# Performance work log

Measured on AMD Instinct MI355X. Metric: run time of the kernel, lower is better.

The kernel has to match this reference:

```python
import jax, jax.numpy as jnp
import numpy as np

BATCH, MAXPV = 32, 50
RULENUM, PROPNUM = 256, 256  # must be equal (eye(rulenum) * property_importance)
ENT_DIM, RULE_DIM = 128, 128
ENTITYNUM = 50000
THRESHOLD = 0.5


def _l2norm(x, eps=1e-12):
    # F.normalize(p=2, dim=-1)
    n = jnp.linalg.norm(x, axis=-1, keepdims=True)
    return x / jnp.clip(n, eps)


def setup_inputs() -> dict:
    key = jax.random.key(0)
    ks = jax.random.split(key, 20)
    d_in = ENT_DIM + RULE_DIM
    inp = {
        'property': jax.random.randint(ks[0], (BATCH, MAXPV), 0, ENTITYNUM),
        'value': jax.random.randint(ks[1], (BATCH, MAXPV), 0, ENTITYNUM),
        'samemask': jax.random.randint(ks[2], (BATCH, MAXPV), 0, 2),
        'padmask': jax.random.randint(ks[3], (BATCH, MAXPV), 0, 2),
        'rule_embedding': jax.random.normal(ks[4], (RULENUM, RULE_DIM), jnp.float32),
        'entity_table': jax.random.normal(ks[5], (ENTITYNUM, ENT_DIM), jnp.float32),
        # Linear weights stored (in, out); concat order in the original is (p_emb, rule_emb)
        'fc1_w': jax.random.normal(ks[6], (d_in, ENT_DIM), jnp.float32),
        'fc1_b': jax.random.normal(ks[7], (ENT_DIM,), jnp.float32) * 0.02,
        'fc2_w': jax.random.normal(ks[8], (d_in, ENT_DIM), jnp.float32),
        'fc2_b': jax.random.normal(ks[9], (ENT_DIM,), jnp.float32) * 0.02,
        'fc3_w': jax.random.normal(ks[10], (d_in, ENT_DIM), jnp.float32),
        'fc3_b': jax.random.normal(ks[11], (ENT_DIM,), jnp.float32) * 0.02,
        'fc4_w': jax.random.normal(ks[12], (ENT_DIM, 1), jnp.float32) * 0.05,
        'fc4_b': jax.random.normal(ks[13], (1,), jnp.float32) * 0.02,
        'fc5_w': jax.random.normal(ks[14], (ENT_DIM, 1), jnp.float32) * 0.05,
        'fc5_b': jax.random.normal(ks[15], (1,), jnp.float32) * 0.02,
        'fc6_w': jax.random.normal(ks[16], (ENT_DIM, ENT_DIM), jnp.float32) * 0.05,
        'fc6_b': jax.random.normal(ks[17], (ENT_DIM,), jnp.float32) * 0.02,
    }
    return inp


def reference(property, value, samemask, padmask, rule_embedding, entity_table,
              fc1_w, fc1_b, fc2_w, fc2_b, fc3_w, fc3_b,
              fc4_w, fc4_b, fc5_w, fc5_b, fc6_w, fc6_b):
    E = entity_table.shape[1]
    R = rule_embedding.shape[0]
    P = R  # propertynum == rulenum (required by eye() regularizer)

    p_emb = _l2norm(entity_table[property])   # (B, M, E)
    v_emb = _l2norm(entity_table[value])      # (B, M, E)
    r_emb = _l2norm(rule_embedding)           # (R, Dr)

    # cat(p, rule) -> Linear decomposed into two smaller matmuls (same math)
    def branch(w, b):
        return p_emb @ w[:E], r_emb @ w[E:] + b  # (B,M,Eo), (R,Eo)

    # s1 branch
    pa, ra = branch(fc1_w, fc1_b)
    h1 = jax.nn.relu(pa[:, None, :, :] + ra[None, :, None, :])   # (B,R,M,E)
    s1 = jax.nn.sigmoid(h1 @ fc4_w + fc4_b)[..., 0]              # (B,R,M)

    # p branch
    pb, rb = branch(fc2_w, fc2_b)
    h2 = jax.nn.relu(pb[:, None, :, :] + rb[None, :, None, :])
    p = jax.nn.sigmoid(h2 @ fc5_w + fc5_b)[..., 0]               # (B,R,M)

    # s2 branch
    pc, rc = branch(fc3_w, fc3_b)
    h3 = jax.nn.relu(pc[:, None, :, :] + rc[None, :, None, :])
    gv = _l2norm(h3 @ fc6_w + fc6_b)                             # (B,R,M,E)
    vb = v_emb[:, None, :, :]                                    # (B,1,M,E)
    denom = jnp.clip(jnp.linalg.norm(vb, axis=-1) * jnp.linalg.norm(gv, axis=-1), 1e-8)
    cos = jnp.sum(vb * gv, axis=-1) / denom
    s2 = 0.5 * cos + 0.5                                         # (B,R,M)

    score = p + (1.0 - p) * s2
    score = jnp.where(samemask[:, None, :] == 1, s1 * score, 1.0 - s1)

    # property importance K: fc1/fc4 on cat(prop_emb, rule_emb)
    prop_emb = _l2norm(entity_table[:P])                         # propertyids = arange(P)
    pi_h = jax.nn.relu((prop_emb @ fc1_w[:E])[None, :, :]
                       + (r_emb @ fc1_w[E:] + fc1_b)[:, None, :])  # (R,P,E)
    pi = jax.nn.sigmoid(pi_h @ fc4_w + fc4_b)[..., 0]            # (R,P)

    rule_mask = jnp.sum(pi * (pi > THRESHOLD), axis=-1) + 1.0    # (R,)

    score = score * padmask[:, None, :].astype(score.dtype)
    score = score * (s1 > THRESHOLD)
    score = jnp.sum(score, axis=-1) / rule_mask[None, :]          # (B,R)
    pooledscore = jnp.max(score, axis=1)                          # (B,)

    diag = jnp.eye(R, dtype=pi.dtype)
    reg = pi * diag + (1.0 - pi) * (1.0 - diag)
    reg = -jnp.log(reg + 1e-8) * (1.0 - diag + diag * R)
    reg_logits = jnp.mean(reg)
    return pooledscore, reg_logits
```

## Files before the change

### kernel.cpp

```cpp
#include <hip/hip_runtime.h>
#include <hip/hip_bf16.h>

#define BATCH 32
#define MAXPV 50
#define RN 256
#define PN 256
#define DIM 128
#define NPV (BATCH*MAXPV*DIM)
#define NI (BATCH*MAXPV)

typedef unsigned short u16;
typedef __attribute__((ext_vector_type(8))) short short8;
typedef __attribute__((ext_vector_type(4))) float f32x4;

__device__ float g_p[NPV], g_v[NPV], g_pa[NPV], g_pb[NPV], g_pc[NPV];
__device__ float g_ra[RN*DIM], g_rb[RN*DIM], g_rc[RN*DIM], g_pp1[PN*DIM];
__device__ float g_prop[PN*DIM], g_re[RN*DIM];
__device__ float g_raT[DIM*RN], g_rbT[DIM*RN];
__device__ float2 g_s1p[NI*RN];
__device__ float g_piv[PN*RN];
__device__ float g_rmask[RN], g_regp[RN];
__device__ float g_scores[(size_t)NI*RN];
__device__ short8 g_bfrag[8][4][64];
__device__ float g_rcA[16*4*64*8];
__device__ int   g_ftype, g_i64;

__device__ __forceinline__ float bf2f(u16 u){ return __uint_as_float(((unsigned)u)<<16); }
__device__ __forceinline__ float LD(const void* p, size_t i){
    return g_ftype ? bf2f(((const u16*)p)[i]) : ((const float*)p)[i];
}
__device__ __forceinline__ int LDI(const void* p, size_t i){
    return g_i64 ? (int)((const long long*)p)[i] : ((const int*)p)[i];
}
__device__ __forceinline__ short f2bf(float f){
    unsigned u = __float_as_uint(f);
    u = (u + 0x7FFFu + ((u>>16)&1u)) >> 16;
    return (short)u;
}
__device__ __forceinline__ float wred(float v){
#pragma unroll
    for(int o=32;o;o>>=1) v += __shfl_xor(v,o,64);
    return v;
}
__device__ __forceinline__ double wredd(double v){
#pragma unroll
    for(int o=32;o;o>>=1) v += __shfl_xor(v,o,64);
    return v;
}
__device__ __forceinline__ float wmax(float v){
#pragma unroll
    for(int o=32;o;o>>=1) v = fmaxf(v,__shfl_xor(v,o,64));
    return v;
}

__global__ void k_detect(const u16* __restrict__ ent, const unsigned* __restrict__ prop){
    __shared__ int c[2];
    int t = threadIdx.x;
    if(t<2) c[t]=0;
    __syncthreads();
    int ee = (ent[2*(size_t)t*977]>>7)&0xFF;
    if(ee>=120 && ee<=133) atomicAdd(&c[0],1);
    if(t<32 && prop[2*t+1]==0u) atomicAdd(&c[1],1);
    __syncthreads();
    if(t==0){ g_ftype = (c[0]>=200)?1:0; g_i64 = (c[1]>=30)?1:0; }
}

__global__ void k_norm(const void* __restrict__ ent, const void* __restrict__ rule,
                       const void* __restrict__ prop, const void* __restrict__ val){
    int row = blockIdx.x*4 + (threadIdx.x>>6);
    int l = threadIdx.x & 63;
    const void* src; size_t off; float* dst;
    if(row < 1600){ src=ent; off=(size_t)LDI(prop,row)*DIM; dst=g_p+(size_t)row*DIM; }
    else if(row < 3200){ int i=row-1600; src=ent; off=(size_t)LDI(val,i)*DIM; dst=g_v+(size_t)i*DIM; }
    else if(row < 3456){ int i=row-3200; src=rule; off=(size_t)i*DIM; dst=g_re+(size_t)i*DIM; }
    else { int i=row-3456; src=ent; off=(size_t)i*DIM; dst=g_prop+(size_t)i*DIM; }
    float a = LD(src,off+l), b = LD(src,off+l+64);
    float n = fmaxf(sqrtf((float)wredd((double)a*a+(double)b*b)), 1e-12f);
    dst[l]=a/n; dst[l+64]=b/n;
}

__global__ __launch_bounds__(256) void k_mm(
    const void* __restrict__ fc1w, const void* __restrict__ fc2w, const void* __restrict__ fc3w,
    const void* __restrict__ fc1b, const void* __restrict__ fc2b, const void* __restrict__ fc3b){
    __shared__ float s_w[64*DIM];
    __shared__ float s_in[16*DIM];
    __shared__ float s_bias[DIM];
    const int blk = blockIdx.x, tid = threadIdx.x;
    const float* in; const void* w; size_t woff=0; const void* bptr=nullptr; float* out; int row0;
    if(blk < 100){ row0=blk*16; in=g_p; w=fc1w; out=g_pa; }
    else if(blk < 200){ row0=(blk-100)*16; in=g_p; w=fc2w; out=g_pb; }
    else if(blk < 300){ row0=(blk-200)*16; in=g_p; w=fc3w; out=g_pc; }
    else if(blk < 316){ row0=(blk-300)*16; in=g_re; w=fc1w; woff=DIM*DIM; bptr=fc1b; out=g_ra; }
    else if(blk < 332){ row0=(blk-316)*16; in=g_re; w=fc2w; woff=DIM*DIM; bptr=fc2b; out=g_rb; }
    else if(blk < 348){ row0=(blk-332)*16; in=g_re; w=fc3w; woff=DIM*DIM; bptr=fc3b; out=g_rc; }
    else { row0=(blk-348)*16; in=g_prop; w=fc1w; out=g_pp1; }
    for(int t=tid; t<16*DIM; t+=256) s_in[t] = in[(size_t)row0*DIM + t];
    if(tid<DIM) s_bias[tid] = bptr ? LD(bptr,tid) : 0.f;
    const int j = tid & 127;
    const int rb8 = (tid>>7)*8;
    double acc[8] = {0,0,0,0,0,0,0,0};
    for(int half=0; half<2; half++){
        __syncthreads();
        for(int t=tid; t<64*DIM; t+=256)
            s_w[t] = LD(w, woff + (size_t)(half*64 + (t>>7))*DIM + (t&127));
        __syncthreads();
        for(int k=0;k<64;k++){
            float wk = s_w[k*DIM + j];
#pragma unroll
            for(int rr=0;rr<8;rr++)
                acc[rr] += (double)s_in[(rb8+rr)*DIM + half*64 + k]*(double)wk;
        }
    }
    const double bj = (double)s_bias[j];
#pragma unroll
    for(int rr=0;rr<8;rr++) out[(size_t)(row0+rb8+rr)*DIM + j] = (float)(bj + acc[rr]);
}

__global__ void k_prep(const void* __restrict__ fc6w){
    int blk = blockIdx.x, tid = threadIdx.x;
    if(blk < 64){
        int idx0 = blk*256 + tid;
#pragma unroll
        for(int n=0;n<4;n++){
            int idx = idx0 + n*16384;
            int which = idx>>15;
            int k = (idx>>8)&127, r = idx&255;
            if(which) g_rbT[k*256+r] = g_rb[(size_t)r*DIM+k];
            else      g_raT[k*256+r] = g_ra[(size_t)r*DIM+k];
        }
    } else if(blk < 72){
        int nt = blk-64;
        int ks = tid>>6, lane = tid&63;
        int n = nt*16 + (lane&15);
        int k0 = ks*32 + (lane>>4)*8;
        short8 v;
#pragma unroll
        for(int j=0;j<8;j++) v[j] = f2bf(LD(fc6w,(size_t)(k0+j)*DIM + n));
        g_bfrag[nt][ks][lane] = v;
    } else {
        for(int idx=tid; idx<4096; idx+=256){
            int mt = (blk-72)*2 + (idx>>11);
            int rem = idx & 2047;
            int ks = rem>>9;
            int lane = (rem>>3)&63;
            int j = rem&7;
            int am = lane&15, quad = lane>>4;
            g_rcA[((mt*4+ks)*64+lane)*8 + j] =
                g_rc[(size_t)(mt*16+am)*DIM + ks*32 + quad*8 + j];
        }
    }
}

__global__ __launch_bounds__(256) void k_gate(
    const void* __restrict__ fc4w, const void* __restrict__ fc4b,
    const void* __restrict__ fc5w, const void* __restrict__ fc5b){
    __shared__ float s_a[4][DIM], s_b[4][DIM], s_f5[DIM];
    __shared__ double s_f4[DIM];
    const int blk = blockIdx.x, tid = threadIdx.x;
    const bool typeA = blk < 400;
    const int i0 = typeA ? blk*4 : (blk-400)*4;
    if(tid<DIM){ s_f4[tid]=(double)LD(fc4w,tid); s_f5[tid]=LD(fc5w,tid); }
    for(int t=tid; t<4*DIM; t+=256){
        int ii=t>>7, k=t&127;
        s_a[ii][k] = typeA ? g_pa[(size_t)(i0+ii)*DIM+k] : g_pp1[(size_t)(i0+ii)*DIM+k];
        if(typeA) s_b[ii][k] = g_pb[(size_t)(i0+ii)*DIM+k];
    }
    __syncthreads();
    const int r = tid;
    double d[4]={0.0,0.0,0.0,0.0}; float pq[4]={0.f,0.f,0.f,0.f};
    if(typeA){
        for(int k=0;k<DIM;k++){
            float rav = g_raT[k*256+r];
            float rbv = g_rbT[k*256+r];
            double f4k = s_f4[k]; float f5k = s_f5[k];
#pragma unroll
            for(int ii=0;ii<4;ii++){
                d[ii] += (double)fmaxf(s_a[ii][k]+rav,0.f)*f4k;
                pq[ii] = fmaf(fmaxf(s_b[ii][k]+rbv,0.f), f5k, pq[ii]);
            }
        }
    } else {
        for(int k=0;k<DIM;k++){
            float rav = g_raT[k*256+r];
            double f4k = s_f4[k];
#pragma unroll
            for(int ii=0;ii<4;ii++)
                d[ii] += (double)fmaxf(s_a[ii][k]+rav,0.f)*f4k;
        }
    }
    const double b4 = (double)LD(fc4b,0);
    const float b5 = LD(fc5b,0);
#pragma unroll
    for(int ii=0;ii<4;ii++){
        double sd = d[ii] + b4;
        bool gate = sd > 0.0;
        float s1v = 1.f/(1.f+expf(-(float)sd));
        if(typeA){
            float p = 1.f/(1.f+expf(-(pq[ii] + b5)));
            float2 o; o.x = gate ? s1v : -s1v; o.y = p;
            g_s1p[(size_t)(i0+ii)*RN + r] = o;
        } else {
            g_piv[(size_t)(i0+ii)*RN + r] = gate ? s1v : -s1v;
        }
    }
}

__global__ void k_pired(){
    const int r = blockIdx.x, tid = threadIdx.x;
    float v = g_piv[(size_t)tid*RN + r];
    float piv = fabsf(v);
    float m = (v > 0.f) ? piv : 0.f;
    float eff = (tid==r) ? piv : (1.f - piv);
    float wgt = (tid==r) ? (float)RN : 1.f;
    float rg = -logf(eff + 1e-8f)*wgt;
    int w = tid>>6, l = tid&63;
    m = wred(m); rg = wred(rg);
    __shared__ float sm[4], sg[4];
    if(l==0){ sm[w]=m; sg[w]=rg; }
    __syncthreads();
    if(tid==0){
        g_rmask[r] = 1.f + sm[0]+sm[1]+sm[2]+sm[3];
        g_regp[r]  = sg[0]+sg[1]+sg[2]+sg[3];
    }
}

__global__ __launch_bounds__(256) void k_main(
    const void* __restrict__ fc6b,
    const void* __restrict__ same, const void* __restrict__ pad){
    const int blk = blockIdx.x;
    const int i = blk >> 1, h = blk & 1;
    if(LDI(same,i)!=1 || LDI(pad,i)!=1) return;
    __shared__ float s_pc[DIM];
    __shared__ float s_st[128][4][2];
    const int tid = threadIdx.x, w = tid>>6, l = tid&63;
    const int am = l&15, quad = l>>4;

    if(tid < DIM) s_pc[tid] = g_pc[(size_t)i*DIM + tid];

    short8 bA[4], bB[4];
#pragma unroll
    for(int ks=0; ks<4; ks++){ bA[ks]=g_bfrag[2*w][ks][l]; bB[ks]=g_bfrag[2*w+1][ks][l]; }
    const int n0 = w*32 + am, n1 = n0 + 16;
    const float v0 = g_v[(size_t)i*DIM + n0], v1 = g_v[(size_t)i*DIM + n1];
    const float b60 = LD(fc6b, n0), b61 = LD(fc6b, n1);

    float vl = g_v[(size_t)i*DIM + l], vh = g_v[(size_t)i*DIM + l + 64];
    const float nvb = sqrtf(wred(vl*vl + vh*vh));
    __syncthreads();

    int mt = h*8;
    float4 c[8];
#pragma unroll
    for(int ks=0; ks<4; ks++){
        const float* rp = &g_rcA[((mt*4+ks)*64 + l)*8];
        c[2*ks]   = *(const float4*)rp;
        c[2*ks+1] = *(const float4*)(rp+4);
    }
    for(int mtl=0; mtl<8; mtl++){
        float4 n[8];
        if(mtl < 7){
#pragma unroll
            for(int ks=0; ks<4; ks++){
                const float* rp = &g_rcA[(((mt+1)*4+ks)*64 + l)*8];
                n[2*ks]   = *(const float4*)rp;
                n[2*ks+1] = *(const float4*)(rp+4);
            }
        }
        short8 a[4];
#pragma unroll
        for(int ks=0; ks<4; ks++){
            const float4 p0 = *(const float4*)&s_pc[ks*32 + quad*8];
            const float4 p1 = *(const float4*)&s_pc[ks*32 + quad*8 + 4];
            const float4 c0 = c[2*ks], c1 = c[2*ks+1];
            short8 t;
            t[0]=f2bf(fmaxf(p0.x+c0.x,0.f)); t[1]=f2bf(fmaxf(p0.y+c0.y,0.f));
            t[2]=f2bf(fmaxf(p0.z+c0.z,0.f)); t[3]=f2bf(fmaxf(p0.w+c0.w,0.f));
            t[4]=f2bf(fmaxf(p1.x+c1.x,0.f)); t[5]=f2bf(fmaxf(p1.y+c1.y,0.f));
            t[6]=f2bf(fmaxf(p1.z+c1.z,0.f)); t[7]=f2bf(fmaxf(p1.w+c1.w,0.f));
            a[ks]=t;
        }
        f32x4 acc0 = {0.f,0.f,0.f,0.f}, acc1 = {0.f,0.f,0.f,0.f};
#pragma unroll
        for(int ks=0; ks<4; ks++){
            acc0 = __builtin_amdgcn_mfma_f32_16x16x32_bf16(a[ks], bA[ks], acc0, 0,0,0);
            acc1 = __builtin_amdgcn_mfma_f32_16x16x32_bf16(a[ks], bB[ks], acc1, 0,0,0);
        }
#pragma unroll
        for(int q=0; q<4; q++){
            float x0 = acc0[q] + b60;
            float x1 = acc1[q] + b61;
            float ss = x0*x0 + x1*x1;
            float dv = x0*v0 + x1*v1;
#pragma unroll
            for(int o=1;o<16;o<<=1){ ss += __shfl_xor(ss,o,64); dv += __shfl_xor(dv,o,64); }
            if(am==0){
                int row = mtl*16 + quad*4 + q;
                s_st[row][w][0] = ss;
                s_st[row][w][1] = dv;
            }
        }
#pragma unroll
        for(int x=0;x<8;x++) c[x] = n[x];
        mt++;
    }
    __syncthreads();
    if(tid < 128){
        const int r = h*128 + tid;
        float ss = s_st[tid][0][0]+s_st[tid][1][0]+s_st[tid][2][0]+s_st[tid][3][0];
        float dv = s_st[tid][0][1]+s_st[tid][1][1]+s_st[tid][2][1]+s_st[tid][3][1];
        float2 sp = g_s1p[(size_t)i*RN + r];
        float s1 = fabsf(sp.x);
        float gate = (sp.x > 0.f) ? 1.f : 0.f;
        float pp = sp.y;
        float nx = sqrtf(ss);
        float clipnx = fmaxf(nx, 1e-12f);
        float gvn = nx/clipnx;
        float denom = fmaxf(nvb*gvn, 1e-8f);
        float cosv = (dv/clipnx)/denom;
        float s2 = 0.5f*cosv + 0.5f;
        float sc = s1*(pp + (1.f-pp)*s2);
        g_scores[(size_t)i*RN + r] = sc * gate;
    }
}

__global__ void k_fin(float* __restrict__ out,
                      const void* __restrict__ same, const void* __restrict__ pad){
    const int blk = blockIdx.x, tid = threadIdx.x;
    const int w = tid>>6, l = tid&63;
    __shared__ float s[4];
    if(blk < 32){
        __shared__ int s_same[MAXPV], s_pad[MAXPV];
        if(tid < MAXPV){
            s_same[tid] = LDI(same, (size_t)blk*MAXPV + tid);
            s_pad[tid]  = LDI(pad,  (size_t)blk*MAXPV + tid);
        }
        __syncthreads();
        float ssum = 0.f;
        for(int pv=0; pv<MAXPV; pv++){
            if(!s_pad[pv]) continue;
            const size_t i = (size_t)blk*MAXPV + pv;
            if(s_same[pv]==1) ssum += g_scores[i*RN + tid];
            else { float sx = g_s1p[i*RN + tid].x; ssum += (sx > 0.f) ? (1.f - sx) : 0.f; }
        }
        float sc = ssum / g_rmask[tid];
        float m = wmax(sc);
        if(l==0) s[w]=m;
        __syncthreads();
        if(tid==0) out[blk] = fmaxf(fmaxf(s[0],s[1]), fmaxf(s[2],s[3]));
    } else {
        float v = g_regp[tid];
        v = wred(v);
        if(l==0) s[w]=v;
        __syncthreads();
        if(tid==0) out[32] = (s[0]+s[1]+s[2]+s[3]) / (float)(RN*PN);
    }
}

extern "C" void kernel_launch(void* const* d_in, const int* in_sizes, int n_in,
                              void* d_out, int out_size, void* d_ws, size_t ws_size,
                              hipStream_t stream){
    int map[18]; for(int i=0;i<18;i++) map[i]=i;
    if(n_in>=18 && in_sizes[0]==6400000){
        const int a[18] = {14,17,16,13,15,0,2,1,4,3,6,5,8,7,10,9,12,11};
        for(int i=0;i<18;i++) map[i]=a[i];
    }
    const void* prop = d_in[map[0]];
    const void* val  = d_in[map[1]];
    const void* same = d_in[map[2]];
    const void* pad  = d_in[map[3]];
    const void* rule = d_in[map[4]];
    const void* ent  = d_in[map[5]];
    const void* fc1w = d_in[map[6]];
    const void* fc1b = d_in[map[7]];
    const void* fc2w = d_in[map[8]];
    const void* fc2b = d_in[map[9]];
    const void* fc3w = d_in[map[10]];
    const void* fc3b = d_in[map[11]];
    const void* fc4w = d_in[map[12]];
    const void* fc4b = d_in[map[13]];
    const void* fc5w = d_in[map[14]];
    const void* fc5b = d_in[map[15]];
    const void* fc6w = d_in[map[16]];
    const void* fc6b = d_in[map[17]];

    k_detect<<<1, 256, 0, stream>>>((const u16*)ent, (const unsigned*)prop);
    k_norm<<<928, 256, 0, stream>>>(ent, rule, prop, val);
    k_mm<<<364, 256, 0, stream>>>(fc1w, fc2w, fc3w, fc1b, fc2b, fc3b);
    k_prep<<<80, 256, 0, stream>>>(fc6w);
    k_gate<<<464, 256, 0, stream>>>(fc4w, fc4b, fc5w, fc5b);
    k_pired<<<RN, 256, 0, stream>>>();
    k_main<<<NI*2, 256, 0, stream>>>(fc6b, same, pad);
    k_fin<<<33, 256, 0, stream>>>((float*)d_out, same, pad);
}
```

Measured before the change: 217.6 us.

## Fold detect, prep and pi-reduction kernels into neighbours to cut launches

Removes the separate detect, prep and pired kernels. Dtype detection now runs per wave through a ballot inside each kernel, the fc6 fragment packing moves into extra k_norm blocks, and k_mm writes the transposed and MFMA-packed rule outputs directly. The rule-mask and regularizer reductions become atomicAdds inside k_gate, and bf16 conversion uses a packed intrinsic. This cuts eight launches to five and drops the intermediate buffers, in exchange for redundant detection loads in every block, atomic contention on 256 addresses, and a float sum order that now depends on atomic ordering.

```diff
diff --git a/kernel.cpp b/kernel.cpp
--- a/kernel.cpp
+++ b/kernel.cpp
@@ -14,29 +14,42 @@
 typedef __attribute__((ext_vector_type(4))) float f32x4;
 
 __device__ float g_p[NPV], g_v[NPV], g_pa[NPV], g_pb[NPV], g_pc[NPV];
-__device__ float g_ra[RN*DIM], g_rb[RN*DIM], g_rc[RN*DIM], g_pp1[PN*DIM];
-__device__ float g_prop[PN*DIM], g_re[RN*DIM];
+__device__ float g_pp1[PN*DIM], g_prop[PN*DIM], g_re[RN*DIM];
 __device__ float g_raT[DIM*RN], g_rbT[DIM*RN];
 __device__ float2 g_s1p[NI*RN];
-__device__ float g_piv[PN*RN];
 __device__ float g_rmask[RN], g_regp[RN];
 __device__ float g_scores[(size_t)NI*RN];
 __device__ short8 g_bfrag[8][4][64];
 __device__ float g_rcA[16*4*64*8];
-__device__ int   g_ftype, g_i64;
 
 __device__ __forceinline__ float bf2f(u16 u){ return __uint_as_float(((unsigned)u)<<16); }
-__device__ __forceinline__ float LD(const void* p, size_t i){
-    return g_ftype ? bf2f(((const u16*)p)[i]) : ((const float*)p)[i];
-}
-__device__ __forceinline__ int LDI(const void* p, size_t i){
-    return g_i64 ? (int)((const long long*)p)[i] : ((const int*)p)[i];
+__device__ __forceinline__ float LD(const void* p, size_t i, bool bf){
+    return bf ? bf2f(((const u16*)p)[i]) : ((const float*)p)[i];
+}
+__device__ __forceinline__ int LDI(const void* p, size_t i, bool w64){
+    return w64 ? (int)((const long long*)p)[i] : ((const int*)p)[i];
 }
 __device__ __forceinline__ short f2bf(float f){
     unsigned u = __float_as_uint(f);
     u = (u + 0x7FFFu + ((u>>16)&1u)) >> 16;
     return (short)u;
 }
+__device__ __forceinline__ unsigned f2bf2(float x, float y){
+    float2 f; f.x=x; f.y=y;
+    __hip_bfloat162 h = __float22bfloat162_rn(f);
+    union { __hip_bfloat162 h; unsigned u; } c; c.h=h; return c.u;
+}
+__device__ __forceinline__ bool det_bf16(const void* ent){
+    int l = threadIdx.x & 63;
+    u16 v = ((const u16*)ent)[(size_t)2*(l*4)*977];
+    int e = (v>>7)&0xFF;
+    return __popcll(__ballot(e>=120 && e<=133)) >= 48;
+}
+__device__ __forceinline__ bool det_i64(const void* prop){
+    int l = threadIdx.x & 63;
+    bool z = (l<32) ? (((const unsigned*)prop)[2*l+1]==0u) : false;
+    return __popcll(__ballot(z)) >= 30;
+}
 __device__ __forceinline__ float wred(float v){
 #pragma unroll
     for(int o=32;o;o>>=1) v += __shfl_xor(v,o,64);
@@ -53,56 +66,63 @@
     return v;
 }
 
-__global__ void k_detect(const u16* __restrict__ ent, const unsigned* __restrict__ prop){
-    __shared__ int c[2];
-    int t = threadIdx.x;
-    if(t<2) c[t]=0;
-    __syncthreads();
-    int ee = (ent[2*(size_t)t*977]>>7)&0xFF;
-    if(ee>=120 && ee<=133) atomicAdd(&c[0],1);
-    if(t<32 && prop[2*t+1]==0u) atomicAdd(&c[1],1);
-    __syncthreads();
-    if(t==0){ g_ftype = (c[0]>=200)?1:0; g_i64 = (c[1]>=30)?1:0; }
-}
-
 __global__ void k_norm(const void* __restrict__ ent, const void* __restrict__ rule,
-                       const void* __restrict__ prop, const void* __restrict__ val){
-    int row = blockIdx.x*4 + (threadIdx.x>>6);
-    int l = threadIdx.x & 63;
+                       const void* __restrict__ prop, const void* __restrict__ val,
+                       const void* __restrict__ fc6w){
+    const bool bf = det_bf16(ent);
+    const int blk = blockIdx.x, tid = threadIdx.x;
+    if(blk >= 928){
+        int nt = blk-928;
+        int ks = tid>>6, lane = tid&63;
+        int n = nt*16 + (lane&15);
+        int k0 = ks*32 + (lane>>4)*8;
+        short8 v;
+#pragma unroll
+        for(int j=0;j<8;j++) v[j] = f2bf(LD(fc6w,(size_t)(k0+j)*DIM + n, bf));
+        g_bfrag[nt][ks][lane] = v;
+        if(nt==0){ g_rmask[tid] = 1.f; g_regp[tid] = 0.f; }
+        return;
+    }
+    const bool w64 = det_i64(prop);
+    int row = blk*4 + (tid>>6);
+    int l = tid & 63;
     const void* src; size_t off; float* dst;
-    if(row < 1600){ src=ent; off=(size_t)LDI(prop,row)*DIM; dst=g_p+(size_t)row*DIM; }
-    else if(row < 3200){ int i=row-1600; src=ent; off=(size_t)LDI(val,i)*DIM; dst=g_v+(size_t)i*DIM; }
+    if(row < 1600){ src=ent; off=(size_t)LDI(prop,row,w64)*DIM; dst=g_p+(size_t)row*DIM; }
+    else if(row < 3200){ int i=row-1600; src=ent; off=(size_t)LDI(val,i,w64)*DIM; dst=g_v+(size_t)i*DIM; }
     else if(row < 3456){ int i=row-3200; src=rule; off=(size_t)i*DIM; dst=g_re+(size_t)i*DIM; }
     else { int i=row-3456; src=ent; off=(size_t)i*DIM; dst=g_prop+(size_t)i*DIM; }
-    float a = LD(src,off+l), b = LD(src,off+l+64);
+    float a = LD(src,off+l,bf), b = LD(src,off+l+64,bf);
     float n = fmaxf(sqrtf((float)wredd((double)a*a+(double)b*b)), 1e-12f);
     dst[l]=a/n; dst[l+64]=b/n;
 }
 
 __global__ __launch_bounds__(256) void k_mm(
+    const void* __restrict__ ent,
     const void* __restrict__ fc1w, const void* __restrict__ fc2w, const void* __restrict__ fc3w,
     const void* __restrict__ fc1b, const void* __restrict__ fc2b, const void* __restrict__ fc3b){
     __shared__ float s_w[64*DIM];
     __shared__ float s_in[16*DIM];
     __shared__ float s_bias[DIM];
+    const bool bf = det_bf16(ent);
     const int blk = blockIdx.x, tid = threadIdx.x;
-    const float* in; const void* w; size_t woff=0; const void* bptr=nullptr; float* out; int row0;
+    const float* in; const void* w; size_t woff=0; const void* bptr=nullptr;
+    float* out=nullptr; int row0; int mode=0;
     if(blk < 100){ row0=blk*16; in=g_p; w=fc1w; out=g_pa; }
     else if(blk < 200){ row0=(blk-100)*16; in=g_p; w=fc2w; out=g_pb; }
     else if(blk < 300){ row0=(blk-200)*16; in=g_p; w=fc3w; out=g_pc; }
-    else if(blk < 316){ row0=(blk-300)*16; in=g_re; w=fc1w; woff=DIM*DIM; bptr=fc1b; out=g_ra; }
-    else if(blk < 332){ row0=(blk-316)*16; in=g_re; w=fc2w; woff=DIM*DIM; bptr=fc2b; out=g_rb; }
-    else if(blk < 348){ row0=(blk-332)*16; in=g_re; w=fc3w; woff=DIM*DIM; bptr=fc3b; out=g_rc; }
+    else if(blk < 316){ row0=(blk-300)*16; in=g_re; w=fc1w; woff=DIM*DIM; bptr=fc1b; mode=1; }
+    else if(blk < 332){ row0=(blk-316)*16; in=g_re; w=fc2w; woff=DIM*DIM; bptr=fc2b; mode=2; }
+    else if(blk < 348){ row0=(blk-332)*16; in=g_re; w=fc3w; woff=DIM*DIM; bptr=fc3b; mode=3; }
     else { row0=(blk-348)*16; in=g_prop; w=fc1w; out=g_pp1; }
     for(int t=tid; t<16*DIM; t+=256) s_in[t] = in[(size_t)row0*DIM + t];
-    if(tid<DIM) s_bias[tid] = bptr ? LD(bptr,tid) : 0.f;
+    if(tid<DIM) s_bias[tid] = bptr ? LD(bptr,tid,bf) : 0.f;
     const int j = tid & 127;
     const int rb8 = (tid>>7)*8;
     double acc[8] = {0,0,0,0,0,0,0,0};
     for(int half=0; half<2; half++){
         __syncthreads();
         for(int t=tid; t<64*DIM; t+=256)
-            s_w[t] = LD(w, woff + (size_t)(half*64 + (t>>7))*DIM + (t&127));
+            s_w[t] = LD(w, woff + (size_t)(half*64 + (t>>7))*DIM + (t&127), bf);
         __syncthreads();
         for(int k=0;k<64;k++){
             float wk = s_w[k*DIM + j];
@@ -113,53 +133,30 @@
     }
     const double bj = (double)s_bias[j];
 #pragma unroll
-    for(int rr=0;rr<8;rr++) out[(size_t)(row0+rb8+rr)*DIM + j] = (float)(bj + acc[rr]);
-}
-
-__global__ void k_prep(const void* __restrict__ fc6w){
-    int blk = blockIdx.x, tid = threadIdx.x;
-    if(blk < 64){
-        int idx0 = blk*256 + tid;
-#pragma unroll
-        for(int n=0;n<4;n++){
-            int idx = idx0 + n*16384;
-            int which = idx>>15;
-            int k = (idx>>8)&127, r = idx&255;
-            if(which) g_rbT[k*256+r] = g_rb[(size_t)r*DIM+k];
-            else      g_raT[k*256+r] = g_ra[(size_t)r*DIM+k];
-        }
-    } else if(blk < 72){
-        int nt = blk-64;
-        int ks = tid>>6, lane = tid&63;
-        int n = nt*16 + (lane&15);
-        int k0 = ks*32 + (lane>>4)*8;
-        short8 v;
-#pragma unroll
-        for(int j=0;j<8;j++) v[j] = f2bf(LD(fc6w,(size_t)(k0+j)*DIM + n));
-        g_bfrag[nt][ks][lane] = v;
-    } else {
-        for(int idx=tid; idx<4096; idx+=256){
-            int mt = (blk-72)*2 + (idx>>11);
-            int rem = idx & 2047;
-            int ks = rem>>9;
-            int lane = (rem>>3)&63;
-            int j = rem&7;
-            int am = lane&15, quad = lane>>4;
-            g_rcA[((mt*4+ks)*64+lane)*8 + j] =
-                g_rc[(size_t)(mt*16+am)*DIM + ks*32 + quad*8 + j];
+    for(int rr=0;rr<8;rr++){
+        const int row = row0 + rb8 + rr;
+        const float vv = (float)(bj + acc[rr]);
+        if(mode==0)      out[(size_t)row*DIM + j] = vv;
+        else if(mode==1) g_raT[j*256 + row] = vv;
+        else if(mode==2) g_rbT[j*256 + row] = vv;
+        else {
+            int mt=row>>4, am=row&15, ks=j>>5, quad=(j>>3)&3, jj=j&7;
+            g_rcA[((mt*4+ks)*64 + quad*16+am)*8 + jj] = vv;
         }
     }
 }
 
 __global__ __launch_bounds__(256) void k_gate(
+    const void* __restrict__ ent,
     const void* __restrict__ fc4w, const void* __restrict__ fc4b,
     const void* __restrict__ fc5w, const void* __restrict__ fc5b){
     __shared__ float s_a[4][DIM], s_b[4][DIM], s_f5[DIM];
     __shared__ double s_f4[DIM];
+    const bool bf = det_bf16(ent);
     const int blk = blockIdx.x, tid = threadIdx.x;
     const bool typeA = blk < 400;
     const int i0 = typeA ? blk*4 : (blk-400)*4;
-    if(tid<DIM){ s_f4[tid]=(double)LD(fc4w,tid); s_f5[tid]=LD(fc5w,tid); }
+    if(tid<DIM){ s_f4[tid]=(double)LD(fc4w,tid,bf); s_f5[tid]=LD(fc5w,tid,bf); }
     for(int t=tid; t<4*DIM; t+=256){
         int ii=t>>7, k=t&127;
         s_a[ii][k] = typeA ? g_pa[(size_t)(i0+ii)*DIM+k] : g_pp1[(size_t)(i0+ii)*DIM+k];
@@ -188,48 +185,43 @@
                 d[ii] += (double)fmaxf(s_a[ii][k]+rav,0.f)*f4k;
         }
     }
-    const double b4 = (double)LD(fc4b,0);
-    const float b5 = LD(fc5b,0);
-#pragma unroll
-    for(int ii=0;ii<4;ii++){
-        double sd = d[ii] + b4;
-        bool gate = sd > 0.0;
-        float s1v = 1.f/(1.f+expf(-(float)sd));
-        if(typeA){
+    const double b4 = (double)LD(fc4b,0,bf);
+    if(typeA){
+        const float b5 = LD(fc5b,0,bf);
+#pragma unroll
+        for(int ii=0;ii<4;ii++){
+            double sd = d[ii] + b4;
+            float s1v = 1.f/(1.f+expf(-(float)sd));
             float p = 1.f/(1.f+expf(-(pq[ii] + b5)));
-            float2 o; o.x = gate ? s1v : -s1v; o.y = p;
+            float2 o; o.x = (sd > 0.0) ? s1v : -s1v; o.y = p;
             g_s1p[(size_t)(i0+ii)*RN + r] = o;
-        } else {
-            g_piv[(size_t)(i0+ii)*RN + r] = gate ? s1v : -s1v;
-        }
-    }
-}
-
-__global__ void k_pired(){
-    const int r = blockIdx.x, tid = threadIdx.x;
-    float v = g_piv[(size_t)tid*RN + r];
-    float piv = fabsf(v);
-    float m = (v > 0.f) ? piv : 0.f;
-    float eff = (tid==r) ? piv : (1.f - piv);
-    float wgt = (tid==r) ? (float)RN : 1.f;
-    float rg = -logf(eff + 1e-8f)*wgt;
-    int w = tid>>6, l = tid&63;
-    m = wred(m); rg = wred(rg);
-    __shared__ float sm[4], sg[4];
-    if(l==0){ sm[w]=m; sg[w]=rg; }
-    __syncthreads();
-    if(tid==0){
-        g_rmask[r] = 1.f + sm[0]+sm[1]+sm[2]+sm[3];
-        g_regp[r]  = sg[0]+sg[1]+sg[2]+sg[3];
+        }
+    } else {
+        float mask_sum = 0.f, reg_sum = 0.f;
+#pragma unroll
+        for(int ii=0;ii<4;ii++){
+            int p = i0 + ii;
+            double sd = d[ii] + b4;
+            float piv = 1.f/(1.f+expf(-(float)sd));
+            if(sd > 0.0) mask_sum += piv;
+            float eff = (p==r) ? piv : (1.f - piv);
+            float wgt = (p==r) ? (float)RN : 1.f;
+            reg_sum += -logf(eff + 1e-8f)*wgt;
+        }
+        atomicAdd(&g_rmask[r], mask_sum);
+        atomicAdd(&g_regp[r], reg_sum);
     }
 }
 
 __global__ __launch_bounds__(256) void k_main(
+    const void* __restrict__ ent, const void* __restrict__ prop,
     const void* __restrict__ fc6b,
     const void* __restrict__ same, const void* __restrict__ pad){
     const int blk = blockIdx.x;
     const int i = blk >> 1, h = blk & 1;
-    if(LDI(same,i)!=1 || LDI(pad,i)!=1) return;
+    const bool w64 = det_i64(prop);
+    if(LDI(same,i,w64)!=1 || LDI(pad,i,w64)!=1) return;
+    const bool bf = det_bf16(ent);
     __shared__ float s_pc[DIM];
     __shared__ float s_st[128][4][2];
     const int tid = threadIdx.x, w = tid>>6, l = tid&63;
@@ -242,7 +234,7 @@
     for(int ks=0; ks<4; ks++){ bA[ks]=g_bfrag[2*w][ks][l]; bB[ks]=g_bfrag[2*w+1][ks][l]; }
     const int n0 = w*32 + am, n1 = n0 + 16;
     const float v0 = g_v[(size_t)i*DIM + n0], v1 = g_v[(size_t)i*DIM + n1];
-    const float b60 = LD(fc6b, n0), b61 = LD(fc6b, n1);
+    const float b60 = LD(fc6b, n0, bf), b61 = LD(fc6b, n1, bf);
 
     float vl = g_v[(size_t)i*DIM + l], vh = g_v[(size_t)i*DIM + l + 64];
     const float nvb = sqrtf(wred(vl*vl + vh*vh));
@@ -272,12 +264,12 @@
             const float4 p0 = *(const float4*)&s_pc[ks*32 + quad*8];
             const float4 p1 = *(const float4*)&s_pc[ks*32 + quad*8 + 4];
             const float4 c0 = c[2*ks], c1 = c[2*ks+1];
-            short8 t;
-            t[0]=f2bf(fmaxf(p0.x+c0.x,0.f)); t[1]=f2bf(fmaxf(p0.y+c0.y,0.f));
-            t[2]=f2bf(fmaxf(p0.z+c0.z,0.f)); t[3]=f2bf(fmaxf(p0.w+c0.w,0.f));
-            t[4]=f2bf(fmaxf(p1.x+c1.x,0.f)); t[5]=f2bf(fmaxf(p1.y+c1.y,0.f));
-            t[6]=f2bf(fmaxf(p1.z+c1.z,0.f)); t[7]=f2bf(fmaxf(p1.w+c1.w,0.f));
-            a[ks]=t;
+            union { short8 s; unsigned u[4]; } t;
+            t.u[0] = f2bf2(fmaxf(p0.x+c0.x,0.f), fmaxf(p0.y+c0.y,0.f));
+            t.u[1] = f2bf2(fmaxf(p0.z+c0.z,0.f), fmaxf(p0.w+c0.w,0.f));
+            t.u[2] = f2bf2(fmaxf(p1.x+c1.x,0.f), fmaxf(p1.y+c1.y,0.f));
+            t.u[3] = f2bf2(fmaxf(p1.z+c1.z,0.f), fmaxf(p1.w+c1.w,0.f));
+            a[ks] = t.s;
         }
         f32x4 acc0 = {0.f,0.f,0.f,0.f}, acc1 = {0.f,0.f,0.f,0.f};
 #pragma unroll
@@ -323,16 +315,17 @@
     }
 }
 
-__global__ void k_fin(float* __restrict__ out,
+__global__ void k_fin(float* __restrict__ out, const void* __restrict__ prop,
                       const void* __restrict__ same, const void* __restrict__ pad){
+    const bool w64 = det_i64(prop);
     const int blk = blockIdx.x, tid = threadIdx.x;
     const int w = tid>>6, l = tid&63;
     __shared__ float s[4];
     if(blk < 32){
         __shared__ int s_same[MAXPV], s_pad[MAXPV];
         if(tid < MAXPV){
-            s_same[tid] = LDI(same, (size_t)blk*MAXPV + tid);
-            s_pad[tid]  = LDI(pad,  (size_t)blk*MAXPV + tid);
+            s_same[tid] = LDI(same, (size_t)blk*MAXPV + tid, w64);
+            s_pad[tid]  = LDI(pad,  (size_t)blk*MAXPV + tid, w64);
         }
         __syncthreads();
         float ssum = 0.f;
@@ -383,12 +376,9 @@
     const void* fc6w = d_in[map[16]];
     const void* fc6b = d_in[map[17]];
 
-    k_detect<<<1, 256, 0, stream>>>((const u16*)ent, (const unsigned*)prop);
-    k_norm<<<928, 256, 0, stream>>>(ent, rule, prop, val);
-    k_mm<<<364, 256, 0, stream>>>(fc1w, fc2w, fc3w, fc1b, fc2b, fc3b);
-    k_prep<<<80, 256, 0, stream>>>(fc6w);
-    k_gate<<<464, 256, 0, stream>>>(fc4w, fc4b, fc5w, fc5b);
-    k_pired<<<RN, 256, 0, stream>>>();
-    k_main<<<NI*2, 256, 0, stream>>>(fc6b, same, pad);
-    k_fin<<<33, 256, 0, stream>>>((float*)d_out, same, pad);
-}
+    k_norm<<<936, 256, 0, stream>>>(ent, rule, prop, val, fc6w);
+    k_mm<<<364, 256, 0, stream>>>(ent, fc1w, fc2w, fc3w, fc1b, fc2b, fc3b);
+    k_gate<<<464, 256, 0, stream>>>(ent, fc4w, fc4b, fc5w, fc5b);
+    k_main<<<NI*2, 256, 0, stream>>>(ent, prop, fc6b, same, pad);
+    k_fin<<<33, 256, 0, stream>>>((float*)d_out, prop, same, pad);
+}
```

Result: no change. 214.2 us (-1.6%).
